# Kernel tuning notes

Measured on AMD Instinct MI355X. Metric: run time of the kernel, lower is better.

The kernel has to match this reference:

```python
import jax, jax.numpy as jnp
import numpy as np

B, N, H, L = 4096, 512, 1024, 8


def setup_inputs() -> dict:
    key = jax.random.key(0)
    k1, k2, k3, k4 = jax.random.split(key, 4)
    x = jax.random.normal(k1, (B, N), dtype=jnp.float32)
    beta = jax.random.uniform(k2, (H, L, N), dtype=jnp.float32)  # torch.rand init
    bound = 1.0 / np.sqrt(N)
    W = jax.random.uniform(k3, (H, N), minval=-bound, maxval=bound, dtype=jnp.float32)
    b = jax.random.uniform(k4, (H,), minval=-bound, maxval=bound, dtype=jnp.float32)
    return {"x": x, "beta": beta, "W": W, "b": b}


def reference(x, beta, W, b):
    # Original computes c[h,j,k] = sum_l beta[h,l,j]*beta[h,l,k], then
    # out_fm[b,h] = sum_{j<k} x[b,j]*x[b,k]*c[h,j,k]  (strict upper-tri mask).
    # FM identity: sum_{j<k} x_j x_k <v_j, v_k>
    #            = 0.5 * sum_l [ (sum_j x_j v_{lj})^2 - sum_j x_j^2 v_{lj}^2 ]
    s = jnp.einsum('bn,hln->bhl', x, beta)            # (B, H, L)
    ssq = jnp.einsum('bn,hln->bhl', x * x, beta * beta)  # (B, H, L)
    fm = 0.5 * jnp.sum(s * s - ssq, axis=-1)          # (B, H)
    linear_out = x @ W.T + b                          # (B, H)
    return fm + linear_out
```

## Files before the change

kernel.cpp:

```cpp
#include <hip/hip_runtime.h>
#include <stdint.h>

static constexpr int B_DIM = 4096;
static constexpr int N_DIM = 512;
static constexpr int H_DIM = 1024;
static constexpr int L_DIM = 8;
static constexpr int HL    = H_DIM * L_DIM;
static constexpr int KC    = 2 * N_DIM;

typedef __attribute__((ext_vector_type(8))) short short8;
typedef __attribute__((ext_vector_type(8))) unsigned short u16x8;
typedef __attribute__((ext_vector_type(4))) float f32x4;

#define BK 64

__device__ __forceinline__ uint16_t f2bf(float f) {
  uint32_t u = __float_as_uint(f);
  u += 0x7fffu + ((u >> 16) & 1u);
  return (uint16_t)(u >> 16);
}

__device__ __forceinline__ void stage16(const uint16_t* g, uint16_t* l) {
  __builtin_amdgcn_global_load_lds(
      (const __attribute__((address_space(1))) void*)g,
      (__attribute__((address_space(3))) void*)l, 16, 0, 0);
}

static constexpr int PREP_T0 = HL * N_DIM / 8;
static constexpr int PREP_T1 = B_DIM * N_DIM / 8;
static constexpr int PREP_T2 = H_DIM * N_DIM / 8;

__global__ void prep_kernel(const float* __restrict__ x, const float* __restrict__ beta,
                            const float* __restrict__ W,
                            uint16_t* __restrict__ xcomb, uint16_t* __restrict__ betab,
                            uint16_t* __restrict__ combW) {
  int t = blockIdx.x * 256 + threadIdx.x;
  if (t < PREP_T0) {
    const f32x4* src = (const f32x4*)(beta + (size_t)t * 8);
    f32x4 a = src[0], b = src[1];
    u16x8 o;
#pragma unroll
    for (int i = 0; i < 4; ++i) { o[i] = f2bf(a[i]); o[4 + i] = f2bf(b[i]); }
    *(u16x8*)(betab + (size_t)t * 8) = o;
    return;
  }
  t -= PREP_T0;
  if (t < PREP_T1) {
    int bb = t >> 6, n8 = (t & 63) * 8;
    const f32x4* src = (const f32x4*)(x + (size_t)bb * N_DIM + n8);
    f32x4 a = src[0], b = src[1];
    u16x8 lo, hi;
#pragma unroll
    for (int i = 0; i < 4; ++i) {
      lo[i] = f2bf(a[i]);     lo[4 + i] = f2bf(b[i]);
      hi[i] = f2bf(a[i] * a[i]); hi[4 + i] = f2bf(b[i] * b[i]);
    }
    *(u16x8*)(xcomb + (size_t)bb * KC + n8)         = lo;
    *(u16x8*)(xcomb + (size_t)bb * KC + N_DIM + n8) = hi;
    return;
  }
  t -= PREP_T1;
  int h = t >> 6, n8 = (t & 63) * 8;
  const f32x4* wsrc = (const f32x4*)(W + (size_t)h * N_DIM + n8);
  f32x4 wa = wsrc[0], wb = wsrc[1];
  u16x8 lo;
#pragma unroll
  for (int i = 0; i < 4; ++i) { lo[i] = f2bf(wa[i]); lo[4 + i] = f2bf(wb[i]); }
  *(u16x8*)(combW + (size_t)h * KC + n8) = lo;
  float s[8] = {};
#pragma unroll
  for (int l = 0; l < L_DIM; ++l) {
    const f32x4* bsrc = (const f32x4*)(beta + ((size_t)h * L_DIM + l) * N_DIM + n8);
    f32x4 a = bsrc[0], b = bsrc[1];
#pragma unroll
    for (int i = 0; i < 4; ++i) { s[i] += a[i] * a[i]; s[4 + i] += b[i] * b[i]; }
  }
  u16x8 hi;
#pragma unroll
  for (int i = 0; i < 8; ++i) hi[i] = f2bf(-0.5f * s[i]);
  *(u16x8*)(combW + (size_t)h * KC + N_DIM + n8) = hi;
}

__global__ __launch_bounds__(256) void fused_gemm_kernel(
    const uint16_t* __restrict__ xcomb,
    const uint16_t* __restrict__ betab,
    const uint16_t* __restrict__ combW,
    const float* __restrict__ bias,
    float* __restrict__ out,
    float* __restrict__ lin)
{
  __shared__ __align__(16) uint16_t As[128 * BK];
  __shared__ __align__(16) uint16_t Bs[128 * BK];

  const int tid  = threadIdx.x;
  const int lane = tid & 63;
  const int wave = tid >> 6;
  const int wm = wave >> 1, wn = wave & 1;
  const int fr   = lane & 15;
  const int quad = lane >> 4;
  const int row0 = blockIdx.y * 128;

  if (blockIdx.x >= 16) {
    const int col0 = (blockIdx.x - 16) * 128;
    f32x4 acc[4][4] = {};
    for (int kt = 0; kt < N_DIM; kt += BK) {
#pragma unroll
      for (int u = 0; u < 4; ++u) {
        int s = tid + u * 256, m = s >> 3, cp = s & 7, c = cp ^ (m & 7);
        stage16(xcomb + (size_t)(row0 + m) * KC + kt + c * 8, As + s * 8);
      }
#pragma unroll
      for (int u = 0; u < 4; ++u) {
        int s = tid + u * 256, m = s >> 3, cp = s & 7, c = cp ^ (m & 7);
        stage16(betab + (size_t)(col0 + m) * N_DIM + kt + c * 8, Bs + s * 8);
      }
      __syncthreads();
#pragma unroll
      for (int kk = 0; kk < BK; kk += 32) {
        short8 af[4], bf[4];
#pragma unroll
        for (int i = 0; i < 4; ++i) {
          int m = wm * 64 + i * 16 + fr;
          int cp = ((kk >> 3) + quad) ^ (m & 7);
          af[i] = *(const short8*)(As + (m * 8 + cp) * 8);
        }
#pragma unroll
        for (int j = 0; j < 4; ++j) {
          int m = wn * 64 + j * 16 + fr;
          int cp = ((kk >> 3) + quad) ^ (m & 7);
          bf[j] = *(const short8*)(Bs + (m * 8 + cp) * 8);
        }
#pragma unroll
        for (int i = 0; i < 4; ++i)
#pragma unroll
          for (int j = 0; j < 4; ++j)
            acc[i][j] = __builtin_amdgcn_mfma_f32_16x16x32_bf16(af[i], bf[j], acc[i][j], 0, 0, 0);
      }
      __syncthreads();
    }
    const int hcol0 = (blockIdx.x - 16) * 16;
#pragma unroll
    for (int i = 0; i < 4; ++i) {
#pragma unroll
      for (int j = 0; j < 4; ++j) {
        const int h_in = wn * 8 + j * 2 + (fr >> 3);
        const int rowb = row0 + wm * 64 + i * 16 + quad * 4;
#pragma unroll
        for (int r = 0; r < 4; ++r) {
          float v = acc[i][j][r];
          v = v * v;
          v += __shfl_xor(v, 1);
          v += __shfl_xor(v, 2);
          v += __shfl_xor(v, 4);
          if ((lane & 7) == 0)
            out[(size_t)(rowb + r) * H_DIM + hcol0 + h_in] = 0.5f * v;
        }
      }
    }
  } else {
    const int col0 = blockIdx.x * 64;
    f32x4 acc[4][2] = {};
    for (int kt = 0; kt < KC; kt += BK) {
#pragma unroll
      for (int u = 0; u < 4; ++u) {
        int s = tid + u * 256, m = s >> 3, cp = s & 7, c = cp ^ (m & 7);
        stage16(xcomb + (size_t)(row0 + m) * KC + kt + c * 8, As + s * 8);
      }
#pragma unroll
      for (int u = 0; u < 2; ++u) {
        int s = tid + u * 256, m = s >> 3, cp = s & 7, c = cp ^ (m & 7);
        stage16(combW + (size_t)(col0 + m) * KC + kt + c * 8, Bs + s * 8);
      }
      __syncthreads();
#pragma unroll
      for (int kk = 0; kk < BK; kk += 32) {
        short8 af[4], bf[2];
#pragma unroll
        for (int i = 0; i < 4; ++i) {
          int m = wm * 64 + i * 16 + fr;
          int cp = ((kk >> 3) + quad) ^ (m & 7);
          af[i] = *(const short8*)(As + (m * 8 + cp) * 8);
        }
#pragma unroll
        for (int j = 0; j < 2; ++j) {
          int m = wn * 32 + j * 16 + fr;
          int cp = ((kk >> 3) + quad) ^ (m & 7);
          bf[j] = *(const short8*)(Bs + (m * 8 + cp) * 8);
        }
#pragma unroll
        for (int i = 0; i < 4; ++i)
#pragma unroll
          for (int j = 0; j < 2; ++j)
            acc[i][j] = __builtin_amdgcn_mfma_f32_16x16x32_bf16(af[i], bf[j], acc[i][j], 0, 0, 0);
      }
      __syncthreads();
    }
#pragma unroll
    for (int i = 0; i < 4; ++i) {
#pragma unroll
      for (int j = 0; j < 2; ++j) {
        const int col  = col0 + wn * 32 + j * 16 + fr;
        const int rowb = row0 + wm * 64 + i * 16 + quad * 4;
        const float bs = bias[col];
#pragma unroll
        for (int r = 0; r < 4; ++r)
          lin[(size_t)(rowb + r) * H_DIM + col] = acc[i][j][r] + bs;
      }
    }
  }
}

__global__ void add_kernel(float* __restrict__ out, const float* __restrict__ lin) {
  int idx = blockIdx.x * 256 + threadIdx.x;
  f32x4 v = ((const f32x4*)lin)[idx];
  f32x4 o = ((f32x4*)out)[idx];
#pragma unroll
  for (int i = 0; i < 4; ++i) o[i] += v[i];
  ((f32x4*)out)[idx] = o;
}

extern "C" void kernel_launch(void* const* d_in, const int* in_sizes, int n_in,
                              void* d_out, int out_size, void* d_ws, size_t ws_size,
                              hipStream_t stream) {
  const float* x    = (const float*)d_in[0];
  const float* beta = (const float*)d_in[1];
  const float* W    = (const float*)d_in[2];
  const float* bias = (const float*)d_in[3];
  float* out = (float*)d_out;

  uint16_t* xcomb = (uint16_t*)d_ws;
  uint16_t* betab = xcomb + (size_t)B_DIM * KC;
  uint16_t* combW = betab + (size_t)HL * N_DIM;
  float*    lin   = (float*)(combW + (size_t)H_DIM * KC);

  const int prep_threads = PREP_T0 + PREP_T1 + PREP_T2;
  prep_kernel<<<prep_threads / 256, 256, 0, stream>>>(x, beta, W, xcomb, betab, combW);

  fused_gemm_kernel<<<dim3(80, 32), 256, 0, stream>>>(xcomb, betab, combW, bias, out, lin);

  add_kernel<<<B_DIM * H_DIM / 4 / 256, 256, 0, stream>>>(out, lin);
}
```

Measured before the change: 178.6 us.

## Fuse linear GEMM into FM blocks and drop separate add kernel

Each FM block now also computes the linear term for its 16 output columns by staging both x and x^2 halves of the A tile plus a small combW tile. The two wave columns split the x and x^2 parts, and the partial sums are combined through LDS. The FM squared result is added in the same place, and the block writes the final output with bias. This removes the intermediate lin buffer, the extra blocks, and the add kernel pass over a 16MB tensor. In exchange it doubles A-tile staging and LDS use per block and adds epilogue synchronisation.

```diff
diff --git a/kernel.cpp b/kernel.cpp
--- a/kernel.cpp
+++ b/kernel.cpp
@@ -11,8 +11,6 @@
 typedef __attribute__((ext_vector_type(8))) short short8;
 typedef __attribute__((ext_vector_type(8))) unsigned short u16x8;
 typedef __attribute__((ext_vector_type(4))) float f32x4;
-
-#define BK 64
 
 __device__ __forceinline__ uint16_t f2bf(float f) {
   uint32_t u = __float_as_uint(f);
@@ -52,7 +50,7 @@
     u16x8 lo, hi;
 #pragma unroll
     for (int i = 0; i < 4; ++i) {
-      lo[i] = f2bf(a[i]);     lo[4 + i] = f2bf(b[i]);
+      lo[i] = f2bf(a[i]);        lo[4 + i] = f2bf(b[i]);
       hi[i] = f2bf(a[i] * a[i]); hi[4 + i] = f2bf(b[i] * b[i]);
     }
     *(u16x8*)(xcomb + (size_t)bb * KC + n8)         = lo;
@@ -81,16 +79,16 @@
   *(u16x8*)(combW + (size_t)h * KC + N_DIM + n8) = hi;
 }
 
-__global__ __launch_bounds__(256) void fused_gemm_kernel(
+__global__ __launch_bounds__(256) void fm_kernel(
     const uint16_t* __restrict__ xcomb,
     const uint16_t* __restrict__ betab,
     const uint16_t* __restrict__ combW,
     const float* __restrict__ bias,
-    float* __restrict__ out,
-    float* __restrict__ lin)
+    float* __restrict__ out)
 {
-  __shared__ __align__(16) uint16_t As[128 * BK];
-  __shared__ __align__(16) uint16_t Bs[128 * BK];
+  __shared__ __align__(16) uint16_t As[128 * 128];
+  __shared__ __align__(16) uint16_t Bs[128 * 64];
+  __shared__ __align__(16) uint16_t Ws[16 * 128];
 
   const int tid  = threadIdx.x;
   const int lane = tid & 63;
@@ -98,125 +96,108 @@
   const int wm = wave >> 1, wn = wave & 1;
   const int fr   = lane & 15;
   const int quad = lane >> 4;
-  const int row0 = blockIdx.y * 128;
-
-  if (blockIdx.x >= 16) {
-    const int col0 = (blockIdx.x - 16) * 128;
-    f32x4 acc[4][4] = {};
-    for (int kt = 0; kt < N_DIM; kt += BK) {
-#pragma unroll
-      for (int u = 0; u < 4; ++u) {
-        int s = tid + u * 256, m = s >> 3, cp = s & 7, c = cp ^ (m & 7);
-        stage16(xcomb + (size_t)(row0 + m) * KC + kt + c * 8, As + s * 8);
-      }
-#pragma unroll
-      for (int u = 0; u < 4; ++u) {
-        int s = tid + u * 256, m = s >> 3, cp = s & 7, c = cp ^ (m & 7);
-        stage16(betab + (size_t)(col0 + m) * N_DIM + kt + c * 8, Bs + s * 8);
-      }
-      __syncthreads();
-#pragma unroll
-      for (int kk = 0; kk < BK; kk += 32) {
-        short8 af[4], bf[4];
+  const int row0  = blockIdx.y * 128;
+  const int col0  = blockIdx.x * 128;
+  const int hcol0 = blockIdx.x * 16;
+
+  f32x4 acc[4][4] = {};
+  f32x4 lacc[4]   = {};
+
+  for (int kt = 0; kt < N_DIM; kt += 64) {
+#pragma unroll
+    for (int u = 0; u < 8; ++u) {
+      int s = tid + u * 256, m = s >> 4, cp = s & 15, c = cp ^ (m & 15);
+      int col = (c >> 3) * N_DIM + kt + (c & 7) * 8;
+      stage16(xcomb + (size_t)(row0 + m) * KC + col, As + s * 8);
+    }
+#pragma unroll
+    for (int u = 0; u < 4; ++u) {
+      int s = tid + u * 256, m = s >> 3, cp = s & 7, c = cp ^ (m & 7);
+      stage16(betab + (size_t)(col0 + m) * N_DIM + kt + c * 8, Bs + s * 8);
+    }
+    {
+      int m = tid >> 4, cp = tid & 15, c = cp ^ m;
+      int col = (c >> 3) * N_DIM + kt + (c & 7) * 8;
+      stage16(combW + (size_t)(hcol0 + m) * KC + col, Ws + tid * 8);
+    }
+    __syncthreads();
+
+#pragma unroll
+    for (int kk2 = 0; kk2 < 2; ++kk2) {
+      const int cbase = kk2 * 4 + quad;
+      short8 af[4], bf[4], al[4], wf;
+#pragma unroll
+      for (int i = 0; i < 4; ++i) {
+        int m = wm * 64 + i * 16 + fr;
+        af[i] = *(const short8*)(As + (m * 16 + (cbase ^ (m & 15))) * 8);
+      }
+#pragma unroll
+      for (int j = 0; j < 4; ++j) {
+        int m = wn * 64 + j * 16 + fr;
+        bf[j] = *(const short8*)(Bs + (m * 8 + (cbase ^ (m & 7))) * 8);
+      }
+      wf = *(const short8*)(Ws + (fr * 16 + ((wn * 8 + cbase) ^ fr)) * 8);
+      if (wn == 0) {
+#pragma unroll
+        for (int i = 0; i < 4; ++i) al[i] = af[i];
+      } else {
 #pragma unroll
         for (int i = 0; i < 4; ++i) {
           int m = wm * 64 + i * 16 + fr;
-          int cp = ((kk >> 3) + quad) ^ (m & 7);
-          af[i] = *(const short8*)(As + (m * 8 + cp) * 8);
+          al[i] = *(const short8*)(As + (m * 16 + ((8 + cbase) ^ (m & 15))) * 8);
         }
-#pragma unroll
-        for (int j = 0; j < 4; ++j) {
-          int m = wn * 64 + j * 16 + fr;
-          int cp = ((kk >> 3) + quad) ^ (m & 7);
-          bf[j] = *(const short8*)(Bs + (m * 8 + cp) * 8);
-        }
-#pragma unroll
-        for (int i = 0; i < 4; ++i)
-#pragma unroll
-          for (int j = 0; j < 4; ++j)
-            acc[i][j] = __builtin_amdgcn_mfma_f32_16x16x32_bf16(af[i], bf[j], acc[i][j], 0, 0, 0);
-      }
-      __syncthreads();
-    }
-    const int hcol0 = (blockIdx.x - 16) * 16;
-#pragma unroll
-    for (int i = 0; i < 4; ++i) {
-#pragma unroll
-      for (int j = 0; j < 4; ++j) {
-        const int h_in = wn * 8 + j * 2 + (fr >> 3);
-        const int rowb = row0 + wm * 64 + i * 16 + quad * 4;
-#pragma unroll
-        for (int r = 0; r < 4; ++r) {
-          float v = acc[i][j][r];
-          v = v * v;
-          v += __shfl_xor(v, 1);
-          v += __shfl_xor(v, 2);
-          v += __shfl_xor(v, 4);
-          if ((lane & 7) == 0)
-            out[(size_t)(rowb + r) * H_DIM + hcol0 + h_in] = 0.5f * v;
-        }
-      }
-    }
-  } else {
-    const int col0 = blockIdx.x * 64;
-    f32x4 acc[4][2] = {};
-    for (int kt = 0; kt < KC; kt += BK) {
-#pragma unroll
-      for (int u = 0; u < 4; ++u) {
-        int s = tid + u * 256, m = s >> 3, cp = s & 7, c = cp ^ (m & 7);
-        stage16(xcomb + (size_t)(row0 + m) * KC + kt + c * 8, As + s * 8);
-      }
-#pragma unroll
-      for (int u = 0; u < 2; ++u) {
-        int s = tid + u * 256, m = s >> 3, cp = s & 7, c = cp ^ (m & 7);
-        stage16(combW + (size_t)(col0 + m) * KC + kt + c * 8, Bs + s * 8);
-      }
-      __syncthreads();
-#pragma unroll
-      for (int kk = 0; kk < BK; kk += 32) {
-        short8 af[4], bf[2];
-#pragma unroll
-        for (int i = 0; i < 4; ++i) {
-          int m = wm * 64 + i * 16 + fr;
-          int cp = ((kk >> 3) + quad) ^ (m & 7);
-          af[i] = *(const short8*)(As + (m * 8 + cp) * 8);
-        }
-#pragma unroll
-        for (int j = 0; j < 2; ++j) {
-          int m = wn * 32 + j * 16 + fr;
-          int cp = ((kk >> 3) + quad) ^ (m & 7);
-          bf[j] = *(const short8*)(Bs + (m * 8 + cp) * 8);
-        }
-#pragma unroll
-        for (int i = 0; i < 4; ++i)
-#pragma unroll
-          for (int j = 0; j < 2; ++j)
-            acc[i][j] = __builtin_amdgcn_mfma_f32_16x16x32_bf16(af[i], bf[j], acc[i][j], 0, 0, 0);
-      }
-      __syncthreads();
-    }
-#pragma unroll
-    for (int i = 0; i < 4; ++i) {
-#pragma unroll
-      for (int j = 0; j < 2; ++j) {
-        const int col  = col0 + wn * 32 + j * 16 + fr;
-        const int rowb = row0 + wm * 64 + i * 16 + quad * 4;
-        const float bs = bias[col];
-#pragma unroll
-        for (int r = 0; r < 4; ++r)
-          lin[(size_t)(rowb + r) * H_DIM + col] = acc[i][j][r] + bs;
-      }
-    }
-  }
-}
-
-__global__ void add_kernel(float* __restrict__ out, const float* __restrict__ lin) {
-  int idx = blockIdx.x * 256 + threadIdx.x;
-  f32x4 v = ((const f32x4*)lin)[idx];
-  f32x4 o = ((f32x4*)out)[idx];
-#pragma unroll
-  for (int i = 0; i < 4; ++i) o[i] += v[i];
-  ((f32x4*)out)[idx] = o;
+      }
+#pragma unroll
+      for (int i = 0; i < 4; ++i)
+#pragma unroll
+        for (int j = 0; j < 4; ++j)
+          acc[i][j] = __builtin_amdgcn_mfma_f32_16x16x32_bf16(af[i], bf[j], acc[i][j], 0, 0, 0);
+#pragma unroll
+      for (int i = 0; i < 4; ++i)
+        lacc[i] = __builtin_amdgcn_mfma_f32_16x16x32_bf16(al[i], wf, lacc[i], 0, 0, 0);
+    }
+    __syncthreads();
+  }
+
+  float* red = (float*)As;
+  if (wn == 0) {
+#pragma unroll
+    for (int i = 0; i < 4; ++i)
+#pragma unroll
+      for (int r = 0; r < 4; ++r)
+        red[(wm * 64 + i * 16 + quad * 4 + r) * 16 + fr] = lacc[i][r];
+  }
+  __syncthreads();
+  if (wn == 1) {
+#pragma unroll
+    for (int i = 0; i < 4; ++i)
+#pragma unroll
+      for (int r = 0; r < 4; ++r)
+        red[(wm * 64 + i * 16 + quad * 4 + r) * 16 + fr] += lacc[i][r];
+  }
+  __syncthreads();
+#pragma unroll
+  for (int i = 0; i < 4; ++i)
+#pragma unroll
+    for (int j = 0; j < 4; ++j) {
+      const int hin = wn * 8 + j * 2 + (fr >> 3);
+#pragma unroll
+      for (int r = 0; r < 4; ++r) {
+        float v = acc[i][j][r];
+        v = v * v;
+        v += __shfl_xor(v, 1);
+        v += __shfl_xor(v, 2);
+        v += __shfl_xor(v, 4);
+        if ((lane & 7) == 0)
+          red[(wm * 64 + i * 16 + quad * 4 + r) * 16 + hin] += 0.5f * v;
+      }
+    }
+  __syncthreads();
+#pragma unroll
+  for (int e = tid; e < 2048; e += 256) {
+    int r = e >> 4, hc = e & 15;
+    out[(size_t)(row0 + r) * H_DIM + hcol0 + hc] = red[e] + bias[hcol0 + hc];
+  }
 }
 
 extern "C" void kernel_launch(void* const* d_in, const int* in_sizes, int n_in,
@@ -231,12 +212,10 @@
   uint16_t* xcomb = (uint16_t*)d_ws;
   uint16_t* betab = xcomb + (size_t)B_DIM * KC;
   uint16_t* combW = betab + (size_t)HL * N_DIM;
-  float*    lin   = (float*)(combW + (size_t)H_DIM * KC);
 
   const int prep_threads = PREP_T0 + PREP_T1 + PREP_T2;
   prep_kernel<<<prep_threads / 256, 256, 0, stream>>>(x, beta, W, xcomb, betab, combW);
 
-  fused_gemm_kernel<<<dim3(80, 32), 256, 0, stream>>>(xcomb, betab, combW, bias, out, lin);
-
-  add_kernel<<<B_DIM * H_DIM / 4 / 256, 256, 0, stream>>>(out, lin);
-}
+  fm_kernel<<<dim3(HL / 128, B_DIM / 128), 256, 0, stream>>>(
+      xcomb, betab, combW, bias, out);
+}
```

Result: faster. 165.0 us (-7.6%).
